# Optimization experiments

Measured on AMD Instinct MI355X. Metric: run time of the kernel, lower is better.

The kernel has to match this reference:

```python
import jax, jax.numpy as jnp
import numpy as np

IMG = 448; P = 16; C = 3; D = 512; DC = 8; DS = 4
NH = IMG // P            # 28 patches per side
NPATCH = NH * NH         # 784
PDIM = C * P * P         # 768
BATCH = 32
EPS = 1e-5


def setup_inputs() -> dict:
    key = jax.random.key(0)
    ks = jax.random.split(key, 10)
    def lin(k, fan_in, shape):
        bound = 1.0 / np.sqrt(fan_in)
        return jax.random.uniform(k, shape, jnp.float32, -bound, bound)
    return {
        "images": jax.random.normal(ks[0], (BATCH, C, IMG, IMG), jnp.float32),
        "W_patch": lin(ks[1], PDIM, (PDIM, D)),
        "b_patch": jnp.zeros((D,), jnp.float32),
        "pos_embed": jax.random.normal(ks[2], (1, NPATCH, D), jnp.float32) * 0.02,
        "W_coord": lin(ks[3], D, (D, DC)),
        "b_coord": jnp.zeros((DC,), jnp.float32),
        "W_spinor": lin(ks[4], D, (D, DS)),
        "b_spinor": jnp.zeros((DS,), jnp.float32),
        "W_embed": lin(ks[5], DC, (DC, D)),
        "b_embed": jnp.zeros((D,), jnp.float32),
        "ln_gamma": jnp.ones((D,), jnp.float32),
        "ln_beta": jnp.zeros((D,), jnp.float32),
        "W_out": lin(ks[6], D, (D, D)),
        "b_out": jnp.zeros((D,), jnp.float32),
    }


def reference(images, W_patch, b_patch, pos_embed, W_coord, b_coord,
              W_spinor, b_spinor, W_embed, b_embed,
              ln_gamma, ln_beta, W_out, b_out):
    B = images.shape[0]
    # patchify == F.unfold(kernel=stride=P).transpose(1,2):
    # patches[b, bh*NH+bw, c*P*P + i*P + j] = images[b, c, bh*P+i, bw*P+j]
    patches = images.reshape(B, C, NH, P, NH, P)
    patches = patches.transpose(0, 2, 4, 1, 3, 5).reshape(B, NPATCH, PDIM)
    # patch embed + positional embedding  -> (B, NPATCH, D)
    x = patches @ W_patch + b_patch + pos_embed
    # manifold projection: coords (B,N,DC), spinor (B,N,DS)
    coords = x @ W_coord + b_coord
    spinor = x @ W_spinor + b_spinor
    # K0 scalar bilinear: psi^T psi -> (B, N)
    K0 = jnp.sum(spinor * spinor, axis=-1)
    # embed back from manifold coords -> (B, N, D)
    x_manifold = coords @ W_embed + b_embed
    # K0-modulated remix + residual
    x_enh = x_manifold * K0[..., None] + x
    # output projection: LayerNorm -> Linear
    mu = jnp.mean(x_enh, axis=-1, keepdims=True)
    var = jnp.mean(jnp.square(x_enh - mu), axis=-1, keepdims=True)
    x_norm = (x_enh - mu) * jax.lax.rsqrt(var + EPS) * ln_gamma + ln_beta
    return x_norm @ W_out + b_out
```

## Files before the change

### kernel.cpp

```cpp
#include <hip/hip_runtime.h>
#include <hip/hip_bf16.h>
#include <stdint.h>


typedef __bf16 bf16_t;
typedef bf16_t bf16x8 __attribute__((ext_vector_type(8)));
typedef bf16_t bf16x4 __attribute__((ext_vector_type(4)));
typedef float  f32x4  __attribute__((ext_vector_type(4)));

#define IMG     448
#define PSZ     16
#define NHP     28
#define NPATCH  784
#define PDIM    768
#define DMODEL  512
#define MROWS   25088

__device__ __forceinline__ void gload16(void* lds, const void* g) {
  __builtin_amdgcn_global_load_lds(
      (__attribute__((address_space(1))) void*)(uintptr_t)g,
      (__attribute__((address_space(3))) void*)lds,
      16, 0, 0);
}

__global__ __launch_bounds__(256) void transpose_to_bf16(
    const float* __restrict__ src, bf16_t* __restrict__ dst, int K, int N)
{
  __shared__ float t[64][65];
  const int tx = threadIdx.x;
  const int ty = threadIdx.y;
  const int bx = blockIdx.x * 64;
  const int by = blockIdx.y * 64;
  #pragma unroll
  for (int r = ty; r < 64; r += 4)
    t[r][tx] = src[(size_t)(by + r) * N + (bx + tx)];
  __syncthreads();
  #pragma unroll
  for (int r = ty; r < 64; r += 4)
    dst[(size_t)(bx + r) * K + (by + tx)] = (bf16_t)t[tx][r];
}

__global__ __launch_bounds__(256) void manifold_prep(
    const float* __restrict__ Wc, const float* __restrict__ Ws,
    bf16_t* __restrict__ Wcsg)
{
  const int idx = blockIdx.x * 256 + threadIdx.x;
  if (idx < 8192) {
    const int r = idx >> 9, n = idx & 511;
    float v = 0.f;
    if (r < 8)       v = Wc[n * 8 + r];
    else if (r < 12) v = Ws[n * 4 + (r - 8)];
    Wcsg[idx] = (bf16_t)v;
  }
}

__global__ __launch_bounds__(256) void patchify_bf16(
    const float* __restrict__ images, bf16_t* __restrict__ Apat)
{
  __shared__ bf16_t t[16][456];
  const int tid = threadIdx.x;
  const int bid = blockIdx.x;
  const int b = bid / 84, rem = bid % 84;
  const int c = rem / 28, ph = rem % 28;
  const float* src = images + ((size_t)(b * 3 + c) * IMG + ph * PSZ) * IMG;

  #pragma unroll
  for (int idx = tid; idx < 16 * 112; idx += 256) {
    const int i = idx / 112, x4 = idx % 112;
    const float4 v = *(const float4*)(src + (size_t)i * IMG + x4 * 4);
    bf16x4 w;
    w[0] = (bf16_t)v.x; w[1] = (bf16_t)v.y; w[2] = (bf16_t)v.z; w[3] = (bf16_t)v.w;
    *(bf16x4*)&t[i][x4 * 4] = w;
  }
  __syncthreads();

  const size_t mbase = (size_t)b * NPATCH + (size_t)ph * NHP;
  #pragma unroll
  for (int idx = tid; idx < 28 * 64; idx += 256) {
    const int pw = idx >> 6, e = idx & 63;
    const int i = e >> 2, j4 = e & 3;
    const bf16x4 w = *(const bf16x4*)&t[i][pw * 16 + j4 * 4];
    *(bf16x4*)&Apat[(mbase + pw) * PDIM + c * 256 + i * 16 + j4 * 4] = w;
  }
}

template<int KDIM, int EPI>
__global__ __launch_bounds__(256) void gemm_bf16(
    const bf16_t* __restrict__ A, const bf16_t* __restrict__ BT,
    const float* __restrict__ bias, const float* __restrict__ pos,
    void* __restrict__ outp)
{
  __shared__ bf16_t As[64 * 64];
  __shared__ bf16_t Bs[128 * 64];
  constexpr int NT = KDIM / 64;

  const int tid  = threadIdx.x;
  const int orig = blockIdx.x;
  const int wg   = (orig & 7) * 196 + (orig >> 3);
  const int n0   = (wg & 3) * 128;
  const int m0   = (wg >> 2) * 64;

  const int wave = tid >> 6, lane = tid & 63;

  const int ra = lane >> 3;
  const int ca = (lane & 7) ^ ra;
  const bf16_t* ag = A  + (size_t)(m0 + wave * 8 + ra) * KDIM + ca * 8;
  const bf16_t* bg = BT + (size_t)(n0 + wave * 8 + ra) * KDIM + ca * 8;
  bf16_t* al0 = As + (wave * 8) * 64;
  bf16_t* al1 = As + (wave * 8 + 32) * 64;
  bf16_t* bl0 = Bs + (wave * 8) * 64;
  bf16_t* bl1 = Bs + (wave * 8 + 32) * 64;
  bf16_t* bl2 = Bs + (wave * 8 + 64) * 64;
  bf16_t* bl3 = Bs + (wave * 8 + 96) * 64;

  const int wm = (wave >> 1) * 32;
  const int wn = (wave & 1) * 64;
  const int lr = lane & 15;
  const int lt = lane >> 4;

  f32x4 acc[2][4] = {};

  for (int t = 0; t < NT; ++t) {
    const int k0 = t * 64;
    __syncthreads();
    gload16(al0, ag + k0);
    gload16(al1, ag + 32 * KDIM + k0);
    gload16(bl0, bg + k0);
    gload16(bl1, bg + 32 * KDIM + k0);
    gload16(bl2, bg + 64 * KDIM + k0);
    gload16(bl3, bg + 96 * KDIM + k0);
    __syncthreads();

    #pragma unroll
    for (int ks = 0; ks < 2; ++ks) {
      const int c = ks * 4 + lt;
      bf16x8 af[2], bfr[4];
      #pragma unroll
      for (int i = 0; i < 2; ++i) {
        const int row = wm + i * 16 + lr;
        af[i] = *(const bf16x8*)&As[row * 64 + ((c ^ (row & 7)) * 8)];
      }
      #pragma unroll
      for (int j = 0; j < 4; ++j) {
        const int row = wn + j * 16 + lr;
        bfr[j] = *(const bf16x8*)&Bs[row * 64 + ((c ^ (row & 7)) * 8)];
      }
      #pragma unroll
      for (int i = 0; i < 2; ++i)
        #pragma unroll
        for (int j = 0; j < 4; ++j)
          acc[i][j] = __builtin_amdgcn_mfma_f32_16x16x32_bf16(af[i], bfr[j], acc[i][j], 0, 0, 0);
    }
  }

  const int q4 = lt << 2;
  const int colb = n0 + wn;
  #pragma unroll
  for (int i = 0; i < 2; ++i) {
    #pragma unroll
    for (int r = 0; r < 4; ++r) {
      const int mm = m0 + wm + i * 16 + q4 + r;
      if (EPI == 0) {
        const int pp = mm % NPATCH;
        const float* pe = pos + (size_t)pp * DMODEL;
        bf16_t* orow = (bf16_t*)outp + (size_t)mm * DMODEL;
        #pragma unroll
        for (int j = 0; j < 4; ++j) {
          const int nn = colb + j * 16 + lr;
          orow[nn] = (bf16_t)(acc[i][j][r] + bias[nn] + pe[nn]);
        }
      } else {
        float* orow = (float*)outp + (size_t)mm * DMODEL;
        #pragma unroll
        for (int j = 0; j < 4; ++j) {
          const int nn = colb + j * 16 + lr;
          orow[nn] = acc[i][j][r] + bias[nn];
        }
      }
    }
  }
}

__global__ __launch_bounds__(256) void gemm1_fused_fallback(
    const float* __restrict__ images, const bf16_t* __restrict__ WpT,
    const float* __restrict__ b_patch, const float* __restrict__ pos_embed,
    bf16_t* __restrict__ xout)
{
  __shared__ bf16_t As[128][40];
  __shared__ bf16_t Bs[128][40];
  const int tid = threadIdx.x;
  const int n0 = blockIdx.x * 128;
  const int m0 = blockIdx.y * 128;
  const int sr = tid >> 1;
  const int sh = tid & 1;
  const int m  = m0 + sr;
  const int b  = m / NPATCH;
  const int p  = m - b * NPATCH;
  const int ph = p / NHP;
  const int pw = p - ph * NHP;
  const float* abase = images + (size_t)(b * 3) * (IMG * IMG)
                              + (size_t)(ph * PSZ) * IMG + pw * PSZ;
  const bf16_t* brow = WpT + (size_t)(n0 + sr) * PDIM + sh * 16;
  const int wave = tid >> 6;
  const int lane = tid & 63;
  const int wm = (wave >> 1) << 6;
  const int wn = (wave & 1) << 6;
  const int lr = lane & 15;
  const int lk = (lane >> 4) << 3;
  f32x4 acc[4][4] = {};
  for (int ks = 0; ks < PDIM / 32; ++ks) {
    const int k0 = ks * 32;
    const int c  = k0 >> 8;
    const int ib = (k0 >> 4) & 15;
    const float* asrc = abase + (size_t)c * (IMG * IMG) + (ib + sh) * IMG;
    const float4 av0 = *(const float4*)(asrc + 0);
    const float4 av1 = *(const float4*)(asrc + 4);
    const float4 av2 = *(const float4*)(asrc + 8);
    const float4 av3 = *(const float4*)(asrc + 12);
    const uint4 bv0 = *(const uint4*)(brow + k0);
    const uint4 bv1 = *(const uint4*)(brow + k0 + 8);
    __syncthreads();
    bf16x8 a0, a1;
    a0[0] = (bf16_t)av0.x; a0[1] = (bf16_t)av0.y; a0[2] = (bf16_t)av0.z; a0[3] = (bf16_t)av0.w;
    a0[4] = (bf16_t)av1.x; a0[5] = (bf16_t)av1.y; a0[6] = (bf16_t)av1.z; a0[7] = (bf16_t)av1.w;
    a1[0] = (bf16_t)av2.x; a1[1] = (bf16_t)av2.y; a1[2] = (bf16_t)av2.z; a1[3] = (bf16_t)av2.w;
    a1[4] = (bf16_t)av3.x; a1[5] = (bf16_t)av3.y; a1[6] = (bf16_t)av3.z; a1[7] = (bf16_t)av3.w;
    *(bf16x8*)&As[sr][sh * 16]     = a0;
    *(bf16x8*)&As[sr][sh * 16 + 8] = a1;
    *(uint4*)&Bs[sr][sh * 16]      = bv0;
    *(uint4*)&Bs[sr][sh * 16 + 8]  = bv1;
    __syncthreads();
    bf16x8 af[4], bfr[4];
    #pragma unroll
    for (int i = 0; i < 4; ++i) af[i]  = *(const bf16x8*)&As[wm + i * 16 + lr][lk];
    #pragma unroll
    for (int j = 0; j < 4; ++j) bfr[j] = *(const bf16x8*)&Bs[wn + j * 16 + lr][lk];
    #pragma unroll
    for (int i = 0; i < 4; ++i)
      #pragma unroll
      for (int j = 0; j < 4; ++j)
        acc[i][j] = __builtin_amdgcn_mfma_f32_16x16x32_bf16(af[i], bfr[j], acc[i][j], 0, 0, 0);
  }
  const int colb = n0 + wn;
  #pragma unroll
  for (int i = 0; i < 4; ++i) {
    #pragma unroll
    for (int r = 0; r < 4; ++r) {
      const int mm = m0 + wm + i * 16 + ((lane >> 4) << 2) + r;
      const int pp = mm % NPATCH;
      const float* pe = pos_embed + (size_t)pp * DMODEL;
      bf16_t* orow = xout + (size_t)mm * DMODEL;
      #pragma unroll
      for (int j = 0; j < 4; ++j) {
        const int nn = colb + j * 16 + lr;
        orow[nn] = (bf16_t)(acc[i][j][r] + b_patch[nn] + pe[nn]);
      }
    }
  }
}

__global__ __launch_bounds__(64) void coords_k0(
    const bf16_t* __restrict__ x, const bf16_t* __restrict__ Wcsg,
    const float* __restrict__ b_coord, const float* __restrict__ b_spinor,
    float* __restrict__ Cbuf)
{
  const int lane = threadIdx.x;
  const int lr   = lane & 15;
  const int lk   = (lane >> 4) << 3;
  const int q4   = (lane >> 4) << 2;
  const int m0w  = blockIdx.x * 16;

  float bbv[4];
  #pragma unroll
  for (int r = 0; r < 4; ++r) {
    if (q4 == 0)      bbv[r] = b_coord[r];
    else if (q4 == 4) bbv[r] = b_coord[4 + r];
    else if (q4 == 8) bbv[r] = b_spinor[r];
    else              bbv[r] = 0.f;
  }

  const bf16_t* xrow = x + (size_t)(m0w + lr) * DMODEL + lk;
  const bf16_t* wrow = Wcsg + lr * DMODEL + lk;
  f32x4 acc1 = {0.f, 0.f, 0.f, 0.f};
  #pragma unroll
  for (int ks = 0; ks < 16; ++ks) {
    const bf16x8 bf = *(const bf16x8*)(xrow + ks * 32);
    const bf16x8 wf = *(const bf16x8*)(wrow + ks * 32);
    acc1 = __builtin_amdgcn_mfma_f32_16x16x32_bf16(wf, bf, acc1, 0, 0, 0);
  }

  float sv[4];
  #pragma unroll
  for (int r = 0; r < 4; ++r) sv[r] = acc1[r] + bbv[r];

  float* crow = Cbuf + (size_t)(m0w + lr) * 12;
  if (q4 == 8) {
    crow[8] = sv[0] * sv[0] + sv[1] * sv[1] + sv[2] * sv[2] + sv[3] * sv[3];
  } else if (q4 == 0 || q4 == 4) {
    f32x4 st = {sv[0], sv[1], sv[2], sv[3]};
    *(f32x4*)(crow + q4) = st;
  }
}

__global__ __launch_bounds__(256) void embed_ln(
    bf16_t* __restrict__ x, const float* __restrict__ Cbuf,
    const float* __restrict__ We, const float* __restrict__ be,
    const float* __restrict__ gamma, const float* __restrict__ beta)
{
  const int w    = threadIdx.x >> 6;
  const int lane = threadIdx.x & 63;
  const int n0   = lane * 8;

  f32x4 wlo[8], whi[8];
  #pragma unroll
  for (int dc = 0; dc < 8; ++dc) {
    wlo[dc] = *(const f32x4*)&We[dc * DMODEL + n0];
    whi[dc] = *(const f32x4*)&We[dc * DMODEL + n0 + 4];
  }
  const f32x4 beL = *(const f32x4*)&be[n0];
  const f32x4 beH = *(const f32x4*)&be[n0 + 4];
  const f32x4 gL  = *(const f32x4*)&gamma[n0];
  const f32x4 gH  = *(const f32x4*)&gamma[n0 + 4];
  const f32x4 btL = *(const f32x4*)&beta[n0];
  const f32x4 btH = *(const f32x4*)&beta[n0 + 4];

  const size_t base = (size_t)blockIdx.x * 32 + w * 8;
  #pragma unroll 2
  for (int rr = 0; rr < 8; ++rr) {
    const size_t row = base + rr;
    const bf16x8 xv = *(const bf16x8*)(x + row * DMODEL + n0);
    const float* crow = Cbuf + row * 12;
    const f32x4 c0 = *(const f32x4*)(crow);
    const f32x4 c1 = *(const f32x4*)(crow + 4);
    const float k0 = crow[8];

    float v[8];
    float s1 = 0.f, s2 = 0.f;
    #pragma unroll
    for (int e = 0; e < 4; ++e) {
      float xm = beL[e];
      #pragma unroll
      for (int dc = 0; dc < 4; ++dc) xm += c0[dc] * wlo[dc][e];
      #pragma unroll
      for (int dc = 0; dc < 4; ++dc) xm += c1[dc] * wlo[4 + dc][e];
      const float vv = xm * k0 + (float)xv[e];
      v[e] = vv; s1 += vv; s2 += vv * vv;
    }
    #pragma unroll
    for (int e = 0; e < 4; ++e) {
      float xm = beH[e];
      #pragma unroll
      for (int dc = 0; dc < 4; ++dc) xm += c0[dc] * whi[dc][e];
      #pragma unroll
      for (int dc = 0; dc < 4; ++dc) xm += c1[dc] * whi[4 + dc][e];
      const float vv = xm * k0 + (float)xv[4 + e];
      v[4 + e] = vv; s1 += vv; s2 += vv * vv;
    }

    #pragma unroll
    for (int off = 1; off <= 32; off <<= 1) {
      s1 += __shfl_xor(s1, off, 64);
      s2 += __shfl_xor(s2, off, 64);
    }
    const float mu  = s1 * (1.f / 512.f);
    const float var = s2 * (1.f / 512.f) - mu * mu;
    const float rs  = rsqrtf(var + 1e-5f);

    bf16x8 o;
    #pragma unroll
    for (int e = 0; e < 4; ++e) {
      o[e]     = (bf16_t)((v[e]     - mu) * rs * gL[e] + btL[e]);
      o[4 + e] = (bf16_t)((v[4 + e] - mu) * rs * gH[e] + btH[e]);
    }
    *(bf16x8*)(x + row * DMODEL + n0) = o;
  }
}

extern "C" void kernel_launch(void* const* d_in, const int* in_sizes, int n_in,
                              void* d_out, int out_size, void* d_ws, size_t ws_size,
                              hipStream_t stream)
{
  const float* images    = (const float*)d_in[0];
  const float* W_patch   = (const float*)d_in[1];
  const float* b_patch   = (const float*)d_in[2];
  const float* pos_embed = (const float*)d_in[3];
  const float* W_coord   = (const float*)d_in[4];
  const float* b_coord   = (const float*)d_in[5];
  const float* W_spinor  = (const float*)d_in[6];
  const float* b_spinor  = (const float*)d_in[7];
  const float* W_embed   = (const float*)d_in[8];
  const float* b_embed   = (const float*)d_in[9];
  const float* ln_gamma  = (const float*)d_in[10];
  const float* ln_beta   = (const float*)d_in[11];
  const float* W_out     = (const float*)d_in[12];
  const float* b_out     = (const float*)d_in[13];
  float* out = (float*)d_out;

  const size_t SZ_APAT = (size_t)MROWS * PDIM * 2;
  const size_t SZ_X    = (size_t)MROWS * DMODEL * 2;
  const size_t SZ_WPT  = (size_t)DMODEL * PDIM * 2;
  const size_t SZ_WOT  = (size_t)DMODEL * DMODEL * 2;
  const size_t SZ_WCS  = 16 * 512 * 2;
  const size_t SZ_CBUF = (size_t)MROWS * 12 * 4;
  const size_t NEED_FULL = SZ_APAT + SZ_X + SZ_WPT + SZ_WOT + SZ_WCS + SZ_CBUF;

  char* ws = (char*)d_ws;
  const bool full = (ws_size >= NEED_FULL);

  bf16_t *Apat, *x, *WpT, *WoT, *Wcsg;
  float *Cbuf;
  if (full) {
    char* p = ws;
    Apat  = (bf16_t*)p;            p += SZ_APAT;
    x     = (bf16_t*)p;            p += SZ_X;
    WpT   = (bf16_t*)p;            p += SZ_WPT;
    WoT   = (bf16_t*)p;            p += SZ_WOT;
    Wcsg  = (bf16_t*)p;            p += SZ_WCS;
    Cbuf  = (float*)p;
  } else {
    char* p = ws;
    Apat  = nullptr;
    x     = (bf16_t*)p;            p += SZ_X;
    WpT   = (bf16_t*)p;            p += SZ_WPT;
    WoT   = (bf16_t*)p;            p += SZ_WOT;
    Wcsg  = (bf16_t*)p;            p += SZ_WCS;
    Cbuf  = (float*)p;
  }

  hipLaunchKernelGGL(transpose_to_bf16, dim3(8, 12), dim3(64, 4), 0, stream,
                     W_patch, WpT, PDIM, DMODEL);
  hipLaunchKernelGGL(transpose_to_bf16, dim3(8, 8), dim3(64, 4), 0, stream,
                     W_out, WoT, DMODEL, DMODEL);
  hipLaunchKernelGGL(manifold_prep, dim3(32), dim3(256), 0, stream,
                     W_coord, W_spinor, Wcsg);

  if (full) {
    hipLaunchKernelGGL(patchify_bf16, dim3(32 * 3 * 28), dim3(256), 0, stream,
                       images, Apat);
    hipLaunchKernelGGL((gemm_bf16<PDIM, 0>), dim3(1568), dim3(256), 0, stream,
                       Apat, WpT, b_patch, pos_embed, (void*)x);
  } else {
    hipLaunchKernelGGL(gemm1_fused_fallback, dim3(4, 196), dim3(256), 0, stream,
                       images, WpT, b_patch, pos_embed, x);
  }

  hipLaunchKernelGGL(coords_k0, dim3(MROWS / 16), dim3(64), 0, stream,
                     x, Wcsg, b_coord, b_spinor, Cbuf);
  hipLaunchKernelGGL(embed_ln, dim3(MROWS / 32), dim3(256), 0, stream,
                     x, Cbuf, W_embed, b_embed, ln_gamma, ln_beta);

  hipLaunchKernelGGL((gemm_bf16<DMODEL, 1>), dim3(1568), dim3(256), 0, stream,
                     x, WoT, b_out, (const float*)nullptr, (void*)out);
}
```

Baseline: 112.6 us.

## Fuse patchify into first GEMM and merge coords with embed-LayerNorm kernel

After: 123.3 us. +9.5%, slower.

```diff
diff --git a/kernel.cpp b/kernel.cpp
--- a/kernel.cpp
+++ b/kernel.cpp
@@ -54,45 +54,14 @@
   }
 }
 
-__global__ __launch_bounds__(256) void patchify_bf16(
-    const float* __restrict__ images, bf16_t* __restrict__ Apat)
-{
-  __shared__ bf16_t t[16][456];
-  const int tid = threadIdx.x;
-  const int bid = blockIdx.x;
-  const int b = bid / 84, rem = bid % 84;
-  const int c = rem / 28, ph = rem % 28;
-  const float* src = images + ((size_t)(b * 3 + c) * IMG + ph * PSZ) * IMG;
-
-  #pragma unroll
-  for (int idx = tid; idx < 16 * 112; idx += 256) {
-    const int i = idx / 112, x4 = idx % 112;
-    const float4 v = *(const float4*)(src + (size_t)i * IMG + x4 * 4);
-    bf16x4 w;
-    w[0] = (bf16_t)v.x; w[1] = (bf16_t)v.y; w[2] = (bf16_t)v.z; w[3] = (bf16_t)v.w;
-    *(bf16x4*)&t[i][x4 * 4] = w;
-  }
-  __syncthreads();
-
-  const size_t mbase = (size_t)b * NPATCH + (size_t)ph * NHP;
-  #pragma unroll
-  for (int idx = tid; idx < 28 * 64; idx += 256) {
-    const int pw = idx >> 6, e = idx & 63;
-    const int i = e >> 2, j4 = e & 3;
-    const bf16x4 w = *(const bf16x4*)&t[i][pw * 16 + j4 * 4];
-    *(bf16x4*)&Apat[(mbase + pw) * PDIM + c * 256 + i * 16 + j4 * 4] = w;
-  }
-}
-
-template<int KDIM, int EPI>
-__global__ __launch_bounds__(256) void gemm_bf16(
-    const bf16_t* __restrict__ A, const bf16_t* __restrict__ BT,
+__global__ __launch_bounds__(256) void gemm1_fused(
+    const float* __restrict__ images, const bf16_t* __restrict__ BT,
     const float* __restrict__ bias, const float* __restrict__ pos,
-    void* __restrict__ outp)
+    bf16_t* __restrict__ outp)
 {
   __shared__ bf16_t As[64 * 64];
   __shared__ bf16_t Bs[128 * 64];
-  constexpr int NT = KDIM / 64;
+  constexpr int NT = PDIM / 64;
 
   const int tid  = threadIdx.x;
   const int orig = blockIdx.x;
@@ -102,6 +71,114 @@
 
   const int wave = tid >> 6, lane = tid & 63;
 
+  const int r_loc = tid >> 2;
+  const int seg   = tid & 3;
+  {
+  }
+  const int m  = m0 + r_loc;
+  const int b  = m / NPATCH;
+  const int p  = m - b * NPATCH;
+  const int ph = p / NHP;
+  const int pw = p - ph * NHP;
+  const float* abase = images + ((size_t)(b * 3) * IMG + ph * PSZ) * IMG + pw * PSZ;
+  bf16_t* aw0 = As + r_loc * 64 + (((2 * seg)     ^ (r_loc & 7)) * 8);
+  bf16_t* aw1 = As + r_loc * 64 + (((2 * seg + 1) ^ (r_loc & 7)) * 8);
+
+  const int ra = lane >> 3;
+  const int ca = (lane & 7) ^ ra;
+  const bf16_t* bg = BT + (size_t)(n0 + wave * 8 + ra) * PDIM + ca * 8;
+  bf16_t* bl0 = Bs + (wave * 8) * 64;
+  bf16_t* bl1 = Bs + (wave * 8 + 32) * 64;
+  bf16_t* bl2 = Bs + (wave * 8 + 64) * 64;
+  bf16_t* bl3 = Bs + (wave * 8 + 96) * 64;
+
+  const int wm = (wave >> 1) * 32;
+  const int wn = (wave & 1) * 64;
+  const int lr = lane & 15;
+  const int lt = lane >> 4;
+
+  f32x4 acc[2][4] = {};
+
+  for (int t = 0; t < NT; ++t) {
+    const int k0 = t * 64;
+    const float* asrc = abase + (size_t)(t >> 2) * (IMG * IMG)
+                              + ((t & 3) * 4 + seg) * IMG;
+    const float4 v0 = *(const float4*)(asrc + 0);
+    const float4 v1 = *(const float4*)(asrc + 4);
+    const float4 v2 = *(const float4*)(asrc + 8);
+    const float4 v3 = *(const float4*)(asrc + 12);
+
+    __syncthreads();
+    bf16x8 w0, w1;
+    w0[0] = (bf16_t)v0.x; w0[1] = (bf16_t)v0.y; w0[2] = (bf16_t)v0.z; w0[3] = (bf16_t)v0.w;
+    w0[4] = (bf16_t)v1.x; w0[5] = (bf16_t)v1.y; w0[6] = (bf16_t)v1.z; w0[7] = (bf16_t)v1.w;
+    w1[0] = (bf16_t)v2.x; w1[1] = (bf16_t)v2.y; w1[2] = (bf16_t)v2.z; w1[3] = (bf16_t)v2.w;
+    w1[4] = (bf16_t)v3.x; w1[5] = (bf16_t)v3.y; w1[6] = (bf16_t)v3.z; w1[7] = (bf16_t)v3.w;
+    *(bf16x8*)aw0 = w0;
+    *(bf16x8*)aw1 = w1;
+    gload16(bl0, bg + k0);
+    gload16(bl1, bg + 32 * PDIM + k0);
+    gload16(bl2, bg + 64 * PDIM + k0);
+    gload16(bl3, bg + 96 * PDIM + k0);
+    __syncthreads();
+
+    #pragma unroll
+    for (int ks = 0; ks < 2; ++ks) {
+      const int c = ks * 4 + lt;
+      bf16x8 af[2], bfr[4];
+      #pragma unroll
+      for (int i = 0; i < 2; ++i) {
+        const int row = wm + i * 16 + lr;
+        af[i] = *(const bf16x8*)&As[row * 64 + ((c ^ (row & 7)) * 8)];
+      }
+      #pragma unroll
+      for (int j = 0; j < 4; ++j) {
+        const int row = wn + j * 16 + lr;
+        bfr[j] = *(const bf16x8*)&Bs[row * 64 + ((c ^ (row & 7)) * 8)];
+      }
+      #pragma unroll
+      for (int i = 0; i < 2; ++i)
+        #pragma unroll
+        for (int j = 0; j < 4; ++j)
+          acc[i][j] = __builtin_amdgcn_mfma_f32_16x16x32_bf16(af[i], bfr[j], acc[i][j], 0, 0, 0);
+    }
+  }
+
+  const int q4 = lt << 2;
+  const int colb = n0 + wn;
+  #pragma unroll
+  for (int i = 0; i < 2; ++i) {
+    #pragma unroll
+    for (int r = 0; r < 4; ++r) {
+      const int mm = m0 + wm + i * 16 + q4 + r;
+      const int pp = mm % NPATCH;
+      const float* pe = pos + (size_t)pp * DMODEL;
+      bf16_t* orow = outp + (size_t)mm * DMODEL;
+      #pragma unroll
+      for (int j = 0; j < 4; ++j) {
+        const int nn = colb + j * 16 + lr;
+        orow[nn] = (bf16_t)(acc[i][j][r] + bias[nn] + pe[nn]);
+      }
+    }
+  }
+}
+
+__global__ __launch_bounds__(256) void gemm2_v5(
+    const bf16_t* __restrict__ A, const bf16_t* __restrict__ BT,
+    const float* __restrict__ bias, float* __restrict__ outp)
+{
+  __shared__ bf16_t As[64 * 64];
+  __shared__ bf16_t Bs[128 * 64];
+  constexpr int KDIM = DMODEL;
+  constexpr int NT = KDIM / 64;
+
+  const int tid  = threadIdx.x;
+  const int orig = blockIdx.x;
+  const int wg   = (orig & 7) * 196 + (orig >> 3);
+  const int n0   = (wg & 3) * 128;
+  const int m0   = (wg >> 2) * 64;
+
+  const int wave = tid >> 6, lane = tid & 63;
   const int ra = lane >> 3;
   const int ca = (lane & 7) ^ ra;
   const bf16_t* ag = A  + (size_t)(m0 + wave * 8 + ra) * KDIM + ca * 8;
@@ -160,110 +237,24 @@
     #pragma unroll
     for (int r = 0; r < 4; ++r) {
       const int mm = m0 + wm + i * 16 + q4 + r;
-      if (EPI == 0) {
-        const int pp = mm % NPATCH;
-        const float* pe = pos + (size_t)pp * DMODEL;
-        bf16_t* orow = (bf16_t*)outp + (size_t)mm * DMODEL;
-        #pragma unroll
-        for (int j = 0; j < 4; ++j) {
-          const int nn = colb + j * 16 + lr;
-          orow[nn] = (bf16_t)(acc[i][j][r] + bias[nn] + pe[nn]);
-        }
-      } else {
-        float* orow = (float*)outp + (size_t)mm * DMODEL;
-        #pragma unroll
-        for (int j = 0; j < 4; ++j) {
-          const int nn = colb + j * 16 + lr;
-          orow[nn] = acc[i][j][r] + bias[nn];
-        }
-      }
-    }
-  }
-}
-
-__global__ __launch_bounds__(256) void gemm1_fused_fallback(
-    const float* __restrict__ images, const bf16_t* __restrict__ WpT,
-    const float* __restrict__ b_patch, const float* __restrict__ pos_embed,
-    bf16_t* __restrict__ xout)
-{
-  __shared__ bf16_t As[128][40];
-  __shared__ bf16_t Bs[128][40];
-  const int tid = threadIdx.x;
-  const int n0 = blockIdx.x * 128;
-  const int m0 = blockIdx.y * 128;
-  const int sr = tid >> 1;
-  const int sh = tid & 1;
-  const int m  = m0 + sr;
-  const int b  = m / NPATCH;
-  const int p  = m - b * NPATCH;
-  const int ph = p / NHP;
-  const int pw = p - ph * NHP;
-  const float* abase = images + (size_t)(b * 3) * (IMG * IMG)
-                              + (size_t)(ph * PSZ) * IMG + pw * PSZ;
-  const bf16_t* brow = WpT + (size_t)(n0 + sr) * PDIM + sh * 16;
-  const int wave = tid >> 6;
-  const int lane = tid & 63;
-  const int wm = (wave >> 1) << 6;
-  const int wn = (wave & 1) << 6;
-  const int lr = lane & 15;
-  const int lk = (lane >> 4) << 3;
-  f32x4 acc[4][4] = {};
-  for (int ks = 0; ks < PDIM / 32; ++ks) {
-    const int k0 = ks * 32;
-    const int c  = k0 >> 8;
-    const int ib = (k0 >> 4) & 15;
-    const float* asrc = abase + (size_t)c * (IMG * IMG) + (ib + sh) * IMG;
-    const float4 av0 = *(const float4*)(asrc + 0);
-    const float4 av1 = *(const float4*)(asrc + 4);
-    const float4 av2 = *(const float4*)(asrc + 8);
-    const float4 av3 = *(const float4*)(asrc + 12);
-    const uint4 bv0 = *(const uint4*)(brow + k0);
-    const uint4 bv1 = *(const uint4*)(brow + k0 + 8);
-    __syncthreads();
-    bf16x8 a0, a1;
-    a0[0] = (bf16_t)av0.x; a0[1] = (bf16_t)av0.y; a0[2] = (bf16_t)av0.z; a0[3] = (bf16_t)av0.w;
-    a0[4] = (bf16_t)av1.x; a0[5] = (bf16_t)av1.y; a0[6] = (bf16_t)av1.z; a0[7] = (bf16_t)av1.w;
-    a1[0] = (bf16_t)av2.x; a1[1] = (bf16_t)av2.y; a1[2] = (bf16_t)av2.z; a1[3] = (bf16_t)av2.w;
-    a1[4] = (bf16_t)av3.x; a1[5] = (bf16_t)av3.y; a1[6] = (bf16_t)av3.z; a1[7] = (bf16_t)av3.w;
-    *(bf16x8*)&As[sr][sh * 16]     = a0;
-    *(bf16x8*)&As[sr][sh * 16 + 8] = a1;
-    *(uint4*)&Bs[sr][sh * 16]      = bv0;
-    *(uint4*)&Bs[sr][sh * 16 + 8]  = bv1;
-    __syncthreads();
-    bf16x8 af[4], bfr[4];
-    #pragma unroll
-    for (int i = 0; i < 4; ++i) af[i]  = *(const bf16x8*)&As[wm + i * 16 + lr][lk];
-    #pragma unroll
-    for (int j = 0; j < 4; ++j) bfr[j] = *(const bf16x8*)&Bs[wn + j * 16 + lr][lk];
-    #pragma unroll
-    for (int i = 0; i < 4; ++i)
-      #pragma unroll
-      for (int j = 0; j < 4; ++j)
-        acc[i][j] = __builtin_amdgcn_mfma_f32_16x16x32_bf16(af[i], bfr[j], acc[i][j], 0, 0, 0);
-  }
-  const int colb = n0 + wn;
-  #pragma unroll
-  for (int i = 0; i < 4; ++i) {
-    #pragma unroll
-    for (int r = 0; r < 4; ++r) {
-      const int mm = m0 + wm + i * 16 + ((lane >> 4) << 2) + r;
-      const int pp = mm % NPATCH;
-      const float* pe = pos_embed + (size_t)pp * DMODEL;
-      bf16_t* orow = xout + (size_t)mm * DMODEL;
+      float* orow = outp + (size_t)mm * DMODEL;
       #pragma unroll
       for (int j = 0; j < 4; ++j) {
         const int nn = colb + j * 16 + lr;
-        orow[nn] = (bf16_t)(acc[i][j][r] + b_patch[nn] + pe[nn]);
-      }
-    }
-  }
-}
-
-__global__ __launch_bounds__(64) void coords_k0(
-    const bf16_t* __restrict__ x, const bf16_t* __restrict__ Wcsg,
+        orow[nn] = acc[i][j][r] + bias[nn];
+      }
+    }
+  }
+}
+
+__global__ __launch_bounds__(64) void manifold_v5(
+    bf16_t* __restrict__ x, const bf16_t* __restrict__ Wcsg,
     const float* __restrict__ b_coord, const float* __restrict__ b_spinor,
-    float* __restrict__ Cbuf)
-{
+    const float* __restrict__ We, const float* __restrict__ be,
+    const float* __restrict__ gamma, const float* __restrict__ beta)
+{
+  __shared__ float cbuf[16][12];
+
   const int lane = threadIdx.x;
   const int lr   = lane & 15;
   const int lk   = (lane >> 4) << 3;
@@ -288,29 +279,19 @@
     const bf16x8 wf = *(const bf16x8*)(wrow + ks * 32);
     acc1 = __builtin_amdgcn_mfma_f32_16x16x32_bf16(wf, bf, acc1, 0, 0, 0);
   }
-
   float sv[4];
   #pragma unroll
   for (int r = 0; r < 4; ++r) sv[r] = acc1[r] + bbv[r];
 
-  float* crow = Cbuf + (size_t)(m0w + lr) * 12;
   if (q4 == 8) {
-    crow[8] = sv[0] * sv[0] + sv[1] * sv[1] + sv[2] * sv[2] + sv[3] * sv[3];
+    cbuf[lr][8] = sv[0] * sv[0] + sv[1] * sv[1] + sv[2] * sv[2] + sv[3] * sv[3];
   } else if (q4 == 0 || q4 == 4) {
     f32x4 st = {sv[0], sv[1], sv[2], sv[3]};
-    *(f32x4*)(crow + q4) = st;
-  }
-}
-
-__global__ __launch_bounds__(256) void embed_ln(
-    bf16_t* __restrict__ x, const float* __restrict__ Cbuf,
-    const float* __restrict__ We, const float* __restrict__ be,
-    const float* __restrict__ gamma, const float* __restrict__ beta)
-{
-  const int w    = threadIdx.x >> 6;
-  const int lane = threadIdx.x & 63;
-  const int n0   = lane * 8;
-
+    *(f32x4*)&cbuf[lr][q4] = st;
+  }
+  __syncthreads();
+
+  const int n0 = lane * 8;
   f32x4 wlo[8], whi[8];
   #pragma unroll
   for (int dc = 0; dc < 8; ++dc) {
@@ -324,15 +305,13 @@
   const f32x4 btL = *(const f32x4*)&beta[n0];
   const f32x4 btH = *(const f32x4*)&beta[n0 + 4];
 
-  const size_t base = (size_t)blockIdx.x * 32 + w * 8;
   #pragma unroll 2
-  for (int rr = 0; rr < 8; ++rr) {
-    const size_t row = base + rr;
+  for (int rr = 0; rr < 16; ++rr) {
+    const size_t row = (size_t)m0w + rr;
     const bf16x8 xv = *(const bf16x8*)(x + row * DMODEL + n0);
-    const float* crow = Cbuf + row * 12;
-    const f32x4 c0 = *(const f32x4*)(crow);
-    const f32x4 c1 = *(const f32x4*)(crow + 4);
-    const float k0 = crow[8];
+    const f32x4 c0 = *(const f32x4*)&cbuf[rr][0];
+    const f32x4 c1 = *(const f32x4*)&cbuf[rr][4];
+    const float k0 = cbuf[rr][8];
 
     float v[8];
     float s1 = 0.f, s2 = 0.f;
@@ -396,36 +375,16 @@
   const float* b_out     = (const float*)d_in[13];
   float* out = (float*)d_out;
 
-  const size_t SZ_APAT = (size_t)MROWS * PDIM * 2;
   const size_t SZ_X    = (size_t)MROWS * DMODEL * 2;
   const size_t SZ_WPT  = (size_t)DMODEL * PDIM * 2;
   const size_t SZ_WOT  = (size_t)DMODEL * DMODEL * 2;
-  const size_t SZ_WCS  = 16 * 512 * 2;
-  const size_t SZ_CBUF = (size_t)MROWS * 12 * 4;
-  const size_t NEED_FULL = SZ_APAT + SZ_X + SZ_WPT + SZ_WOT + SZ_WCS + SZ_CBUF;
 
   char* ws = (char*)d_ws;
-  const bool full = (ws_size >= NEED_FULL);
-
-  bf16_t *Apat, *x, *WpT, *WoT, *Wcsg;
-  float *Cbuf;
-  if (full) {
-    char* p = ws;
-    Apat  = (bf16_t*)p;            p += SZ_APAT;
-    x     = (bf16_t*)p;            p += SZ_X;
-    WpT   = (bf16_t*)p;            p += SZ_WPT;
-    WoT   = (bf16_t*)p;            p += SZ_WOT;
-    Wcsg  = (bf16_t*)p;            p += SZ_WCS;
-    Cbuf  = (float*)p;
-  } else {
-    char* p = ws;
-    Apat  = nullptr;
-    x     = (bf16_t*)p;            p += SZ_X;
-    WpT   = (bf16_t*)p;            p += SZ_WPT;
-    WoT   = (bf16_t*)p;            p += SZ_WOT;
-    Wcsg  = (bf16_t*)p;            p += SZ_WCS;
-    Cbuf  = (float*)p;
-  }
+  char* p  = ws;
+  bf16_t* x    = (bf16_t*)p;   p += SZ_X;
+  bf16_t* WpT  = (bf16_t*)p;   p += SZ_WPT;
+  bf16_t* WoT  = (bf16_t*)p;   p += SZ_WOT;
+  bf16_t* Wcsg = (bf16_t*)p;
 
   hipLaunchKernelGGL(transpose_to_bf16, dim3(8, 12), dim3(64, 4), 0, stream,
                      W_patch, WpT, PDIM, DMODEL);
@@ -434,21 +393,12 @@
   hipLaunchKernelGGL(manifold_prep, dim3(32), dim3(256), 0, stream,
                      W_coord, W_spinor, Wcsg);
 
-  if (full) {
-    hipLaunchKernelGGL(patchify_bf16, dim3(32 * 3 * 28), dim3(256), 0, stream,
-                       images, Apat);
-    hipLaunchKernelGGL((gemm_bf16<PDIM, 0>), dim3(1568), dim3(256), 0, stream,
-                       Apat, WpT, b_patch, pos_embed, (void*)x);
-  } else {
-    hipLaunchKernelGGL(gemm1_fused_fallback, dim3(4, 196), dim3(256), 0, stream,
-                       images, WpT, b_patch, pos_embed, x);
-  }
-
-  hipLaunchKernelGGL(coords_k0, dim3(MROWS / 16), dim3(64), 0, stream,
-                     x, Wcsg, b_coord, b_spinor, Cbuf);
-  hipLaunchKernelGGL(embed_ln, dim3(MROWS / 32), dim3(256), 0, stream,
-                     x, Cbuf, W_embed, b_embed, ln_gamma, ln_beta);
-
-  hipLaunchKernelGGL((gemm_bf16<DMODEL, 1>), dim3(1568), dim3(256), 0, stream,
-                     x, WoT, b_out, (const float*)nullptr, (void*)out);
-}
+  hipLaunchKernelGGL(gemm1_fused, dim3(1568), dim3(256), 0, stream,
+                     images, WpT, b_patch, pos_embed, x);
+
+  hipLaunchKernelGGL(manifold_v5, dim3(MROWS / 16), dim3(64), 0, stream,
+                     x, Wcsg, b_coord, b_spinor, W_embed, b_embed, ln_gamma, ln_beta);
+
+  hipLaunchKernelGGL(gemm2_v5, dim3(1568), dim3(256), 0, stream,
+                     x, WoT, b_out, out);
+}
```
